# Performance work log

Measured on AMD Instinct MI355X. Metric: run time of the kernel, lower is better.

Reference implementation:

```python
import jax, jax.numpy as jnp
import numpy as np

N_NODES, N_EDGES = 50000, 800000
IN, HID, HEADS, OUT = 128, 64, 4, 64


def _segment_softmax(e, seg, n):
    # softmax over edges grouped by source node (torch.sparse.softmax dim=1), per head
    m = jax.ops.segment_max(e, seg, num_segments=n)
    ex = jnp.exp(e - m[seg])
    s = jax.ops.segment_sum(ex, seg, num_segments=n)
    return ex / s[seg]


def _attention_layer(x, src, dst, lw, lb, aw, ab, final):
    n = x.shape[0]
    h = jax.nn.leaky_relu(x @ lw.T + lb, 0.2)            # (N, F)
    f = h.shape[1]
    # Faithful decomposition of Conv1d(2*F*H, H, k=1, groups=H) applied to
    # concat([tile(h_i, H), tile(h_j, H)]): group k covers tiled copies 2k and 2k+1;
    # copies < H come from h_i (src), copies >= H from h_j (dst).
    k = jnp.arange(HEADS)
    sel1 = (2 * k < HEADS).astype(h.dtype)[:, None]       # first half of group weights
    sel2 = (2 * k + 1 < HEADS).astype(h.dtype)[:, None]   # second half
    Wi = aw[:, :f] * sel1 + aw[:, f:] * sel2              # (H, F) acting on h_src
    Wj = aw[:, :f] * (1.0 - sel1) + aw[:, f:] * (1.0 - sel2)  # (H, F) acting on h_dst
    e = (h @ Wi.T)[src] + (h @ Wj.T)[dst] + ab            # (E, H)
    alpha = _segment_softmax(e, src, n)                   # (E, H)
    # h2[i] = sum_{j in N(i)} h[j] outer alpha[ij]  -> (N, F, H)
    h2 = jax.ops.segment_sum(h[dst][:, :, None] * alpha[:, None, :], src, num_segments=n)
    if final:
        return jax.nn.relu(h2.mean(axis=-1))              # (N, OUT)
    return jax.nn.relu(h2.reshape(n, -1))                 # (N, F*H)


def setup_inputs() -> dict:
    key = jax.random.key(0)
    ks = jax.random.split(key, 16)
    d = {}
    d["x"] = jax.random.normal(ks[0], (N_NODES, IN), jnp.float32)
    dims_in = [IN, HID * HEADS, HID * HEADS]
    dims_out = [HID, HID, OUT]
    i = 1
    for L in range(3):
        di, do = dims_in[L], dims_out[L]
        d[f"lin{L}_w"] = jax.random.normal(ks[i], (do, di), jnp.float32) / np.float32(np.sqrt(di)); i += 1
        d[f"lin{L}_b"] = jax.random.normal(ks[i], (do,), jnp.float32) * 0.01; i += 1
        d[f"att{L}_w"] = jax.random.normal(ks[i], (HEADS, 2 * do), jnp.float32) / np.float32(np.sqrt(2 * do)); i += 1
        d[f"att{L}_b"] = jax.random.normal(ks[i], (HEADS,), jnp.float32) * 0.01; i += 1
    d["src"] = jnp.sort(jax.random.randint(ks[13], (N_EDGES,), 0, N_NODES, dtype=jnp.int32))
    d["dst"] = jax.random.randint(ks[14], (N_EDGES,), 0, N_NODES, dtype=jnp.int32)
    return d


def reference(x, lin0_w, lin0_b, att0_w, att0_b, lin1_w, lin1_b, att1_w, att1_b,
              lin2_w, lin2_b, att2_w, att2_b, src, dst):
    layers = [(lin0_w, lin0_b, att0_w, att0_b),
              (lin1_w, lin1_b, att1_w, att1_b),
              (lin2_w, lin2_b, att2_w, att2_b)]
    out = x
    for i, (lw, lb, aw, ab) in enumerate(layers):
        out = _attention_layer(out, src, dst, lw, lb, aw, ab, final=(i == len(layers) - 1))
    return out
```

## Files before the change

### kernel.cpp

```cpp
#include <hip/hip_runtime.h>
#include <hip/hip_fp16.h>

#define N_NODES 50000
#define N_EDGES 800000

typedef _Float16 half8 __attribute__((ext_vector_type(8)));
typedef _Float16 f16x4 __attribute__((ext_vector_type(4)));
typedef float floatx4 __attribute__((ext_vector_type(4)));

__global__ __launch_bounds__(256) void setup_kernel(const int* __restrict__ src,
                                                    int* __restrict__ row_ptr,
                                                    const float* __restrict__ lw0,
                                                    const float* __restrict__ lw1,
                                                    const float* __restrict__ lw2,
                                                    _Float16* __restrict__ w0p,
                                                    _Float16* __restrict__ w1p,
                                                    _Float16* __restrict__ w2p) {
    int idx = blockIdx.x * 256 + threadIdx.x;
    if (blockIdx.y == 0) {
        if (idx > N_NODES) return;
        int lo = 0, hi = N_EDGES;
        while (lo < hi) {
            int mid = (lo + hi) >> 1;
            if (src[mid] < idx) lo = mid + 1; else hi = mid;
        }
        row_ptr[idx] = lo;
        return;
    }
    if (blockIdx.y == 1) {
        if (idx < 64 * 128) w0p[idx] = (_Float16)lw0[idx];
        return;
    }
    if (idx >= 64 * 192) return;
    int o = idx / 192, r = idx % 192;
    int ch = r >> 6, f = r & 63;
    const float* lw = (blockIdx.y == 2) ? lw1 : lw2;
    float v;
    if (ch == 0)      v = lw[o * 256 + f * 4 + 0] + lw[o * 256 + f * 4 + 1];
    else if (ch == 1) v = lw[o * 256 + f * 4 + 2];
    else              v = lw[o * 256 + f * 4 + 3];
    (blockIdx.y == 2 ? w1p : w2p)[idx] = (_Float16)v;
}

template <typename TIn, int K>
__global__ __launch_bounds__(256) void lin_kernel(const TIn* __restrict__ in,
                                                  const _Float16* __restrict__ w,
                                                  const float* __restrict__ b,
                                                  const float* __restrict__ aw,
                                                  _Float16* __restrict__ h,
                                                  float2* __restrict__ s, int n) {
    const int t = threadIdx.x;
    const int l = t & 63;
    const int wv = t >> 6;
    const int arow = l & 15;
    const int kg = l >> 4;
    const long rowbase = (long)blockIdx.x * 64 + wv * 16;
    long arow_g = rowbase + arow;
    if (arow_g >= n) arow_g = n - 1;

    floatx4 acc[4] = {};

    for (int kc = 0; kc < K; kc += 32) {
        const int ks = kc + kg * 8;
        half8 a;
        if (sizeof(TIn) == 4) {
            const TIn* ap = in + arow_g * K + ks;
            #pragma unroll
            for (int j = 0; j < 8; ++j) a[j] = (_Float16)ap[j];
        } else {
            a = *(const half8*)((const _Float16*)in + arow_g * K + ks);
        }
        #pragma unroll
        for (int ct = 0; ct < 4; ++ct) {
            half8 bb = *(const half8*)(w + (long)(ct * 16 + arow) * K + ks);
            acc[ct] = __builtin_amdgcn_mfma_f32_16x16x32_f16(a, bb, acc[ct], 0, 0, 0);
        }
    }

    const int c = l & 15;
    const int rq = l >> 4;
    float bias[4], a2c[4], a3c[4];
    #pragma unroll
    for (int ct = 0; ct < 4; ++ct) {
        int col = ct * 16 + c;
        bias[ct] = b[col];
        a2c[ct] = aw[2 * 128 + col] + aw[2 * 128 + 64 + col];
        a3c[ct] = aw[3 * 128 + col] + aw[3 * 128 + 64 + col];
    }
    #pragma unroll
    for (int r = 0; r < 4; ++r) {
        long row = rowbase + rq * 4 + r;
        bool ok = row < n;
        float q2 = 0.f, q3 = 0.f;
        _Float16 hv[4];
        #pragma unroll
        for (int ct = 0; ct < 4; ++ct) {
            float u = acc[ct][r] + bias[ct];
            u = u > 0.f ? u : 0.2f * u;
            q2 += u * a2c[ct];
            q3 += u * a3c[ct];
            hv[ct] = (_Float16)u;
        }
        if (ok) {
            #pragma unroll
            for (int ct = 0; ct < 4; ++ct) h[row * 64 + ct * 16 + c] = hv[ct];
        }
        #pragma unroll
        for (int o = 1; o < 16; o <<= 1) {
            q2 += __shfl_xor(q2, o);
            q3 += __shfl_xor(q3, o);
        }
        if (c == 0 && ok) s[row] = make_float2(__expf(q2), __expf(q3));
    }
}

__global__ __launch_bounds__(256) void agg_kernel(const _Float16* __restrict__ hfeat,
                                                  const float2* __restrict__ E,
                                                  const int* __restrict__ dst,
                                                  const int* __restrict__ row_ptr,
                                                  _Float16* __restrict__ out_h,
                                                  float* __restrict__ out_f,
                                                  int final_layer, int n) {
    const int t = threadIdx.x;
    const int l = t & 63;
    const int i = blockIdx.x * 4 + (t >> 6);
    if (i >= n) return;
    const int r0 = row_ptr[i], r1 = row_ptr[i + 1];
    const int deg = r1 - r0;
    const int q = l >> 4;
    const int fl = l & 15;

    if (deg == 0) {
        if (!final_layer) {
            if (q < 3) *(f16x4*)(out_h + (long)i * 192 + q * 64 + fl * 4) =
                f16x4{(_Float16)0.f, (_Float16)0.f, (_Float16)0.f, (_Float16)0.f};
        } else if (q == 0) {
            *(floatx4*)(out_f + (long)i * 64 + fl * 4) = floatx4{0.f, 0.f, 0.f, 0.f};
        }
        return;
    }

    float am[4] = {}, a2[4] = {}, a3[4] = {};
    float S2 = 0.f, S3 = 0.f;

    for (int c0 = r0; c0 < r1; c0 += 64) {
        const int cn = min(64, r1 - c0);
        const int dl = dst[c0 + min(l, cn - 1)];

        for (int jj = 0; jj < cn; jj += 16) {
            int dg[4]; float vg[4];
            #pragma unroll
            for (int g = 0; g < 4; ++g) {
                int e = jj + g * 4 + q;
                int ec = e < cn ? e : cn - 1;
                dg[g] = __shfl(dl, ec);
                vg[g] = e < cn ? 1.f : 0.f;
            }
            f16x4 hv[4]; float2 Ev[4];
            #pragma unroll
            for (int g = 0; g < 4; ++g) {
                hv[g] = *(const f16x4*)(hfeat + (long)dg[g] * 64 + fl * 4);
                Ev[g] = E[dg[g]];
            }
            #pragma unroll
            for (int g = 0; g < 4; ++g) {
                float vm = vg[g];
                float e2 = vm * Ev[g].x, e3 = vm * Ev[g].y;
                S2 += e2; S3 += e3;
                #pragma unroll
                for (int k = 0; k < 4; ++k) {
                    float hf = (float)hv[g][k];
                    am[k] += vm * hf;
                    a2[k] += e2 * hf;
                    a3[k] += e3 * hf;
                }
            }
        }
    }

    #pragma unroll
    for (int o = 16; o < 64; o <<= 1) {
        #pragma unroll
        for (int k = 0; k < 4; ++k) {
            am[k] += __shfl_xor(am[k], o);
            a2[k] += __shfl_xor(a2[k], o);
            a3[k] += __shfl_xor(a3[k], o);
        }
        S2 += __shfl_xor(S2, o);
        S3 += __shfl_xor(S3, o);
    }

    const float inv_deg = 1.f / (float)deg;
    const float i2 = 1.f / S2, i3 = 1.f / S3;

    if (!final_layer) {
        if (q == 0) {
            f16x4 o0, o1, o2;
            #pragma unroll
            for (int k = 0; k < 4; ++k) {
                o0[k] = (_Float16)fmaxf(am[k] * inv_deg, 0.f);
                o1[k] = (_Float16)fmaxf(a2[k] * i2, 0.f);
                o2[k] = (_Float16)fmaxf(a3[k] * i3, 0.f);
            }
            *(f16x4*)(out_h + (long)i * 192 + fl * 4)       = o0;
            *(f16x4*)(out_h + (long)i * 192 + 64 + fl * 4)  = o1;
            *(f16x4*)(out_h + (long)i * 192 + 128 + fl * 4) = o2;
        }
    } else {
        if (q == 0) {
            floatx4 o;
            #pragma unroll
            for (int k = 0; k < 4; ++k)
                o[k] = fmaxf(0.5f * inv_deg * am[k] + 0.25f * (a2[k] * i2 + a3[k] * i3), 0.f);
            *(floatx4*)(out_f + (long)i * 64 + fl * 4) = o;
        }
    }
}

extern "C" void kernel_launch(void* const* d_in, const int* in_sizes, int n_in,
                              void* d_out, int out_size, void* d_ws, size_t ws_size,
                              hipStream_t stream) {
    const float* x = (const float*)d_in[0];
    const float* lw[3] = {(const float*)d_in[1], (const float*)d_in[5], (const float*)d_in[9]};
    const float* lb[3] = {(const float*)d_in[2], (const float*)d_in[6], (const float*)d_in[10]};
    const float* aw[3] = {(const float*)d_in[3], (const float*)d_in[7], (const float*)d_in[11]};
    const int* src = (const int*)d_in[13];
    const int* dst = (const int*)d_in[14];
    float* out = (float*)d_out;

    const int N = N_NODES;

    _Float16* hA = (_Float16*)d_ws;
    _Float16* hB = hA + (size_t)N * 64;
    _Float16* g  = hB + (size_t)N * 64;
    float2* sA = (float2*)(g + (size_t)N * 192);
    float2* sB = sA + N;
    _Float16* w0p = (_Float16*)(sB + N);
    _Float16* w1p = w0p + 64 * 128;
    _Float16* w2p = w1p + 64 * 192;
    int* row_ptr = (int*)(w2p + 64 * 192);

    const int lin_grid = (N + 63) / 64;
    const int node_grid = (N + 3) / 4;

    setup_kernel<<<dim3(196, 4), 256, 0, stream>>>(src, row_ptr, lw[0], lw[1], lw[2],
                                                   w0p, w1p, w2p);

    lin_kernel<float, 128><<<lin_grid, 256, 0, stream>>>(x, w0p, lb[0], aw[0], hA, sA, N);

    agg_kernel<<<node_grid, 256, 0, stream>>>(hA, sA, dst, row_ptr, g, out, 0, N);
    lin_kernel<_Float16, 192><<<lin_grid, 256, 0, stream>>>(g, w1p, lb[1], aw[1], hB, sB, N);

    agg_kernel<<<node_grid, 256, 0, stream>>>(hB, sB, dst, row_ptr, g, out, 0, N);
    lin_kernel<_Float16, 192><<<lin_grid, 256, 0, stream>>>(g, w2p, lb[2], aw[2], hA, sA, N);

    agg_kernel<<<node_grid, 256, 0, stream>>>(hA, sA, dst, row_ptr, g, out, 1, N);
}
```

Before: 234.4 us.

## Fuse neighbor aggregation with next layer's linear MFMA in one kernel

```diff
diff --git a/kernel.cpp b/kernel.cpp
--- a/kernel.cpp
+++ b/kernel.cpp
@@ -114,47 +114,48 @@
     }
 }
 
-__global__ __launch_bounds__(256) void agg_kernel(const _Float16* __restrict__ hfeat,
-                                                  const float2* __restrict__ E,
-                                                  const int* __restrict__ dst,
-                                                  const int* __restrict__ row_ptr,
-                                                  _Float16* __restrict__ out_h,
-                                                  float* __restrict__ out_f,
-                                                  int final_layer, int n) {
+template <int FINAL>
+__global__ __launch_bounds__(256) void layer_kernel(const _Float16* __restrict__ hfeat,
+                                                    const float2* __restrict__ E,
+                                                    const int* __restrict__ dst,
+                                                    const int* __restrict__ row_ptr,
+                                                    const _Float16* __restrict__ w,
+                                                    const float* __restrict__ b,
+                                                    const float* __restrict__ aw,
+                                                    _Float16* __restrict__ h_out,
+                                                    float2* __restrict__ s_out,
+                                                    float* __restrict__ out_f) {
+    __shared__ _Float16 g_lds[16][200];
+    __shared__ float2 spart[4][16];
+
     const int t = threadIdx.x;
     const int l = t & 63;
-    const int i = blockIdx.x * 4 + (t >> 6);
-    if (i >= n) return;
-    const int r0 = row_ptr[i], r1 = row_ptr[i + 1];
-    const int deg = r1 - r0;
+    const int wv = t >> 6;
     const int q = l >> 4;
     const int fl = l & 15;
-
-    if (deg == 0) {
-        if (!final_layer) {
-            if (q < 3) *(f16x4*)(out_h + (long)i * 192 + q * 64 + fl * 4) =
-                f16x4{(_Float16)0.f, (_Float16)0.f, (_Float16)0.f, (_Float16)0.f};
-        } else if (q == 0) {
-            *(floatx4*)(out_f + (long)i * 64 + fl * 4) = floatx4{0.f, 0.f, 0.f, 0.f};
-        }
-        return;
-    }
+    const int base = blockIdx.x * 16;
+    const int i = base + wv * 4 + q;
+
+    const int r0 = row_ptr[i];
+    const int deg = row_ptr[i + 1] - r0;
+    int md = deg;
+    md = max(md, __shfl_xor(md, 16));
+    md = max(md, __shfl_xor(md, 32));
 
     float am[4] = {}, a2[4] = {}, a3[4] = {};
     float S2 = 0.f, S3 = 0.f;
-
-    for (int c0 = r0; c0 < r1; c0 += 64) {
-        const int cn = min(64, r1 - c0);
-        const int dl = dst[c0 + min(l, cn - 1)];
-
-        for (int jj = 0; jj < cn; jj += 16) {
-            int dg[4]; float vg[4];
+    const int safew = deg > 0 ? r0 + deg - 1 : 0;
+
+    for (int c0 = 0; c0 < md; c0 += 16) {
+        const int dl = dst[min(r0 + c0 + fl, safew)];
+        const int jn = min(16, md - c0);
+        for (int j = 0; j < jn; j += 4) {
+            int dg[4]; float vm[4];
             #pragma unroll
             for (int g = 0; g < 4; ++g) {
-                int e = jj + g * 4 + q;
-                int ec = e < cn ? e : cn - 1;
-                dg[g] = __shfl(dl, ec);
-                vg[g] = e < cn ? 1.f : 0.f;
+                const int sl = j + g;
+                dg[g] = __shfl(dl, (q << 4) | sl);
+                vm[g] = (c0 + sl < deg) ? 1.f : 0.f;
             }
             f16x4 hv[4]; float2 Ev[4];
             #pragma unroll
@@ -164,13 +165,12 @@
             }
             #pragma unroll
             for (int g = 0; g < 4; ++g) {
-                float vm = vg[g];
-                float e2 = vm * Ev[g].x, e3 = vm * Ev[g].y;
+                const float e2 = vm[g] * Ev[g].x, e3 = vm[g] * Ev[g].y;
                 S2 += e2; S3 += e3;
                 #pragma unroll
                 for (int k = 0; k < 4; ++k) {
-                    float hf = (float)hv[g][k];
-                    am[k] += vm * hf;
+                    const float hf = (float)hv[g][k];
+                    am[k] += vm[g] * hf;
                     a2[k] += e2 * hf;
                     a3[k] += e3 * hf;
                 }
@@ -178,42 +178,66 @@
         }
     }
 
-    #pragma unroll
-    for (int o = 16; o < 64; o <<= 1) {
+    const float inv_deg = deg > 0 ? 1.f / (float)deg : 0.f;
+    const float i2 = deg > 0 ? 1.f / S2 : 0.f;
+    const float i3 = deg > 0 ? 1.f / S3 : 0.f;
+
+    if (FINAL) {
+        floatx4 o;
+        #pragma unroll
+        for (int k = 0; k < 4; ++k)
+            o[k] = fmaxf(0.5f * inv_deg * am[k] + 0.25f * (a2[k] * i2 + a3[k] * i3), 0.f);
+        *(floatx4*)(out_f + (long)i * 64 + fl * 4) = o;
+        return;
+    }
+
+    {
+        const int nl = wv * 4 + q;
+        f16x4 o0, o1, o2;
         #pragma unroll
         for (int k = 0; k < 4; ++k) {
-            am[k] += __shfl_xor(am[k], o);
-            a2[k] += __shfl_xor(a2[k], o);
-            a3[k] += __shfl_xor(a3[k], o);
-        }
-        S2 += __shfl_xor(S2, o);
-        S3 += __shfl_xor(S3, o);
-    }
-
-    const float inv_deg = 1.f / (float)deg;
-    const float i2 = 1.f / S2, i3 = 1.f / S3;
-
-    if (!final_layer) {
-        if (q == 0) {
-            f16x4 o0, o1, o2;
-            #pragma unroll
-            for (int k = 0; k < 4; ++k) {
-                o0[k] = (_Float16)fmaxf(am[k] * inv_deg, 0.f);
-                o1[k] = (_Float16)fmaxf(a2[k] * i2, 0.f);
-                o2[k] = (_Float16)fmaxf(a3[k] * i3, 0.f);
-            }
-            *(f16x4*)(out_h + (long)i * 192 + fl * 4)       = o0;
-            *(f16x4*)(out_h + (long)i * 192 + 64 + fl * 4)  = o1;
-            *(f16x4*)(out_h + (long)i * 192 + 128 + fl * 4) = o2;
-        }
-    } else {
-        if (q == 0) {
-            floatx4 o;
-            #pragma unroll
-            for (int k = 0; k < 4; ++k)
-                o[k] = fmaxf(0.5f * inv_deg * am[k] + 0.25f * (a2[k] * i2 + a3[k] * i3), 0.f);
-            *(floatx4*)(out_f + (long)i * 64 + fl * 4) = o;
-        }
+            o0[k] = (_Float16)fmaxf(am[k] * inv_deg, 0.f);
+            o1[k] = (_Float16)fmaxf(a2[k] * i2, 0.f);
+            o2[k] = (_Float16)fmaxf(a3[k] * i3, 0.f);
+        }
+        *(f16x4*)(&g_lds[nl][fl * 4])       = o0;
+        *(f16x4*)(&g_lds[nl][64 + fl * 4])  = o1;
+        *(f16x4*)(&g_lds[nl][128 + fl * 4]) = o2;
+    }
+    __syncthreads();
+
+    floatx4 acc = {};
+    #pragma unroll
+    for (int kc = 0; kc < 192; kc += 32) {
+        const int ks = kc + q * 8;
+        half8 a = *(const half8*)(&g_lds[fl][ks]);
+        half8 bb = *(const half8*)(w + (long)(wv * 16 + fl) * 192 + ks);
+        acc = __builtin_amdgcn_mfma_f32_16x16x32_f16(a, bb, acc, 0, 0, 0);
+    }
+
+    const int col = wv * 16 + fl;
+    const float bias = b[col];
+    const float a2c = aw[2 * 128 + col] + aw[2 * 128 + 64 + col];
+    const float a3c = aw[3 * 128 + col] + aw[3 * 128 + 64 + col];
+    #pragma unroll
+    for (int r = 0; r < 4; ++r) {
+        const int row = q * 4 + r;
+        float u = acc[r] + bias;
+        u = u > 0.f ? u : 0.2f * u;
+        h_out[(long)(base + row) * 64 + col] = (_Float16)u;
+        float q2 = u * a2c, q3 = u * a3c;
+        #pragma unroll
+        for (int o = 1; o < 16; o <<= 1) {
+            q2 += __shfl_xor(q2, o);
+            q3 += __shfl_xor(q3, o);
+        }
+        if (fl == 0) spart[wv][row] = make_float2(q2, q3);
+    }
+    __syncthreads();
+    if (t < 16) {
+        const float2 p0 = spart[0][t], p1 = spart[1][t], p2 = spart[2][t], p3 = spart[3][t];
+        s_out[base + t] = make_float2(__expf(p0.x + p1.x + p2.x + p3.x),
+                                      __expf(p0.y + p1.y + p2.y + p3.y));
     }
 }
 
@@ -232,8 +256,7 @@
 
     _Float16* hA = (_Float16*)d_ws;
     _Float16* hB = hA + (size_t)N * 64;
-    _Float16* g  = hB + (size_t)N * 64;
-    float2* sA = (float2*)(g + (size_t)N * 192);
+    float2* sA = (float2*)(hB + (size_t)N * 64);
     float2* sB = sA + N;
     _Float16* w0p = (_Float16*)(sB + N);
     _Float16* w1p = w0p + 64 * 128;
@@ -241,18 +264,19 @@
     int* row_ptr = (int*)(w2p + 64 * 192);
 
     const int lin_grid = (N + 63) / 64;
-    const int node_grid = (N + 3) / 4;
+    const int layer_grid = N / 16;
 
     setup_kernel<<<dim3(196, 4), 256, 0, stream>>>(src, row_ptr, lw[0], lw[1], lw[2],
                                                    w0p, w1p, w2p);
 
     lin_kernel<float, 128><<<lin_grid, 256, 0, stream>>>(x, w0p, lb[0], aw[0], hA, sA, N);
 
-    agg_kernel<<<node_grid, 256, 0, stream>>>(hA, sA, dst, row_ptr, g, out, 0, N);
-    lin_kernel<_Float16, 192><<<lin_grid, 256, 0, stream>>>(g, w1p, lb[1], aw[1], hB, sB, N);
-
-    agg_kernel<<<node_grid, 256, 0, stream>>>(hB, sB, dst, row_ptr, g, out, 0, N);
-    lin_kernel<_Float16, 192><<<lin_grid, 256, 0, stream>>>(g, w2p, lb[2], aw[2], hA, sA, N);
-
-    agg_kernel<<<node_grid, 256, 0, stream>>>(hA, sA, dst, row_ptr, g, out, 1, N);
-}
+    layer_kernel<0><<<layer_grid, 256, 0, stream>>>(hA, sA, dst, row_ptr,
+                                                    w1p, lb[1], aw[1], hB, sB, out);
+
+    layer_kernel<0><<<layer_grid, 256, 0, stream>>>(hB, sB, dst, row_ptr,
+                                                    w2p, lb[2], aw[2], hA, sA, out);
+
+    layer_kernel<1><<<layer_grid, 256, 0, stream>>>(hA, sA, dst, row_ptr,
+                                                    w2p, lb[2], aw[2], hB, sB, out);
+}
```

Result: faster. 199.9 us (-14.7%).
